# Kernel tuning notes

Hardware: AMD Instinct MI355X
Metric: run time of the kernel (lower is better)

The kernel has to match this reference:

```python
import jax, jax.numpy as jnp
import numpy as np

V, K, C, F = 100000, 64, 3, 16
HID = [64, 64, 64]  # 'large' pca-net hidden widths (config.yaml stand-in)
EPS = 1e-4


def setup_inputs() -> dict:
    key = jax.random.key(0)
    ks = jax.random.split(key, 12)
    inp = {
        "coordinates": jax.random.normal(ks[0], (V, C), jnp.float32),
        "distsq": jax.random.uniform(ks[1], (V, K), jnp.float32),
        "features": jax.random.uniform(ks[2], (V, F), jnp.float32),
        "n_idxs": jax.random.randint(ks[3], (V, K), 0, V, jnp.int32),
    }
    dims = [C * C] + HID + [C * C]
    for i in range(len(dims) - 1):
        fan_in = dims[i]
        inp[f"W{i}"] = jax.random.normal(ks[4 + 2 * i], (dims[i], dims[i + 1]), jnp.float32) / np.sqrt(fan_in)
        inp[f"b{i}"] = jnp.zeros((dims[i + 1],), jnp.float32)
    return inp


def _neighbour_covariance(coordinates, distsq, features, n_idxs):
    # gather neighbour coords/features: [V,K,C], [V,K,F]
    nbc = jnp.take(coordinates, n_idxs, axis=0)
    nbf = jnp.take(features, n_idxs, axis=0)
    # per-neighbour per-feature weights, distsq pre-scaled by 10 in call()
    w = nbf * jnp.exp(-10.0 * distsq)[:, :, None]          # [V,K,F]
    wsum = jnp.sum(w, axis=1) + EPS                         # [V,F]
    mean = jnp.einsum("vkf,vkc->vfc", w, nbc) / wsum[:, :, None]  # [V,F,C]
    # E[x x^T] - mu mu^T (avoids materializing [V,K,F,C] centered diffs)
    m2 = jnp.einsum("vkf,vkc,vkd->vfcd", w, nbc, nbc) / wsum[:, :, None, None]
    cov = m2 - mean[:, :, :, None] * mean[:, :, None, :]    # [V,F,C,C]
    return cov, mean


def reference(coordinates, distsq, features, n_idxs,
              W0, b0, W1, b1, W2, b2, W3, b3):
    cov, mean = _neighbour_covariance(coordinates, distsq, features, n_idxs)
    x = cov.reshape(-1, C * C)                              # [V*F, C^2]
    # per-layer path: ELU on every layer, including the final one
    for Wl, bl in ((W0, b0), (W1, b1), (W2, b2), (W3, b3)):
        x = jax.nn.elu(x @ Wl + bl)
    return x.reshape(-1, F * C * C)                         # [V, F*C^2]
```

## Files before the change

### kernel.cpp

```cpp
#include <hip/hip_runtime.h>
#include <hip/hip_bf16.h>
#include <math.h>

#define NV 100000
#define NK 64
#define NF 16
#define EPS_W 1e-4f
#define WS_NEED ((size_t)NV * 16 * 32)
#define GRID_MLP 3125

typedef __attribute__((ext_vector_type(8))) short bf16x8;
typedef __attribute__((ext_vector_type(4))) float f32x4;

__device__ __forceinline__ unsigned short bfu(float x) {
    return __builtin_bit_cast(unsigned short, (__bf16)x);
}
__device__ __forceinline__ unsigned int pk2(float lo, float hi) {
    float2 t; t.x = lo; t.y = hi;
    __hip_bfloat162 r = __float22bfloat162_rn(t);
    unsigned int u;
    __builtin_memcpy(&u, &r, 4);
    return u;
}
__device__ __forceinline__ float eluf(float x) {
    return x > 0.f ? x : __expf(x) - 1.f;
}

__launch_bounds__(256)
__global__ void cov_kernel(const float* __restrict__ coords,
                           const float* __restrict__ distsq,
                           const float* __restrict__ feats,
                           const int*   __restrict__ nidx,
                           unsigned char* __restrict__ ws)
{
    __shared__ float sEW[16][64];
    __shared__ int   sIX[16][64];
    const int tid = threadIdx.x;
    const int gv  = tid >> 4;
    const int f   = tid & 15;
    const int v   = blockIdx.x * 16 + gv;

    {
        const size_t base = (size_t)v * NK + 4 * f;
        float4 d4 = *(const float4*)(distsq + base);
        int4   i4 = *(const int4*)(nidx + base);
        sEW[gv][4*f+0] = __expf(-10.f * d4.x);
        sEW[gv][4*f+1] = __expf(-10.f * d4.y);
        sEW[gv][4*f+2] = __expf(-10.f * d4.z);
        sEW[gv][4*f+3] = __expf(-10.f * d4.w);
        sIX[gv][4*f+0] = i4.x; sIX[gv][4*f+1] = i4.y;
        sIX[gv][4*f+2] = i4.z; sIX[gv][4*f+3] = i4.w;
    }
    __syncthreads();

    float s = 0.f, m0=0.f,m1=0.f,m2=0.f;
    float q00=0.f,q01=0.f,q02=0.f,q11=0.f,q12=0.f,q22=0.f;

    #pragma unroll 8
    for (int k = 0; k < NK; ++k) {
        int   idx = sIX[gv][k];
        float ew  = sEW[gv][k];
        float w   = feats[(size_t)idx * NF + f] * ew;
        float x = coords[(size_t)idx*3+0];
        float y = coords[(size_t)idx*3+1];
        float z = coords[(size_t)idx*3+2];
        s += w;
        m0 = fmaf(w,x,m0); m1 = fmaf(w,y,m1); m2 = fmaf(w,z,m2);
        float wx=w*x, wy=w*y, wz=w*z;
        q00=fmaf(wx,x,q00); q01=fmaf(wx,y,q01); q02=fmaf(wx,z,q02);
        q11=fmaf(wy,y,q11); q12=fmaf(wy,z,q12); q22=fmaf(wz,z,q22);
    }
    float inv = 1.f / (s + EPS_W);
    float mu0=m0*inv, mu1=m1*inv, mu2=m2*inv;
    float c00=fmaf(-mu0,mu0,q00*inv);
    float c01=fmaf(-mu0,mu1,q01*inv);
    float c02=fmaf(-mu0,mu2,q02*inv);
    float c11=fmaf(-mu1,mu1,q11*inv);
    float c12=fmaf(-mu1,mu2,q12*inv);
    float c22=fmaf(-mu2,mu2,q22*inv);

    uint4 lo, hi;
    lo.x = pk2(c00, c01);
    lo.y = pk2(c02, c01);
    lo.z = pk2(c11, c12);
    lo.w = pk2(c02, c12);
    hi.x = pk2(c22, 1.0f);
    hi.y = 0u; hi.z = 0u; hi.w = 0u;

    uint4* dst = (uint4*)(ws + ((size_t)v * 16 + f) * 32);
    dst[0] = lo;
    dst[1] = hi;
}

__device__ __forceinline__ bf16x8 rdfrag(const short* hb, int c, int g, int kc) {
    int boff = ((kc << 6) + (g << 4)) ^ ((c & 7) << 4);
    return *(const bf16x8*)(hb + c * 64 + (boff >> 1));
}
__device__ __forceinline__ void wrH(short* hb, int c, int g, int t,
                                    unsigned int p01, unsigned int p23) {
    int boff = ((t << 5) + (g << 3)) ^ ((c & 7) << 4);
    uint2 val; val.x = p01; val.y = p23;
    *(uint2*)(hb + c * 64 + (boff >> 1)) = val;
}
__device__ __forceinline__ bf16x8 rdW(const short* sw, int c, int g, int t, int kc) {
    int byte = (t << 11) + (c << 7) + (kc << 6) + (g << 4);
    byte ^= (c & 7) << 4;
    return *(const bf16x8*)((const char*)sw + byte);
}

__launch_bounds__(256, 4)
__global__ void mlp5b_kernel(const unsigned char* __restrict__ ws,
                             const float* __restrict__ W0, const float* __restrict__ b0,
                             const float* __restrict__ W1, const float* __restrict__ b1,
                             const float* __restrict__ W2, const float* __restrict__ b2,
                             const float* __restrict__ W3, const float* __restrict__ b3,
                             float* __restrict__ out)
{
    __shared__ __align__(16) short sW1[4096];
    __shared__ __align__(16) short sW2[4096];
    __shared__ __align__(16) short hbuf[4][1024];

    const int tid  = threadIdx.x;
    const int wid  = tid >> 6;
    const int lane = tid & 63;
    const int c    = lane & 15;
    const int g    = lane >> 4;

    union U8 { short s[8]; bf16x8 v; };

    #pragma unroll
    for (int r = 0; r < 2; ++r) {
        int t = tid + r * 256;
        int j = t & 63, o = t >> 6;
        U8 u1, u2;
        #pragma unroll
        for (int i = 0; i < 8; ++i) {
            u1.s[i] = (short)bfu(W1[(8 * o + i) * 64 + j]);
            u2.s[i] = (short)bfu(W2[(8 * o + i) * 64 + j]);
        }
        int byte = ((j << 7) + (o << 4)) ^ ((j & 7) << 4);
        *(bf16x8*)((char*)sW1 + byte) = u1.v;
        *(bf16x8*)((char*)sW2 + byte) = u2.v;
    }
    __syncthreads();

    bf16x8 w0f[4], w3f[2];
    #pragma unroll
    for (int t = 0; t < 4; ++t) {
        U8 u;
        #pragma unroll
        for (int i = 0; i < 8; ++i) {
            int k = 8 * g + i;
            float val = 0.f;
            if (k < 9)       val = W0[k * 64 + 16 * t + c];
            else if (k == 9) val = b0[16 * t + c];
            u.s[i] = (short)bfu(val);
        }
        w0f[t] = u.v;
    }
    #pragma unroll
    for (int kc = 0; kc < 2; ++kc) {
        U8 u;
        #pragma unroll
        for (int i = 0; i < 8; ++i) {
            int k = 32 * kc + 8 * g + i;
            u.s[i] = (short)bfu(c < 9 ? W3[k * 9 + c] : 0.f);
        }
        w3f[kc] = u.v;
    }
    float b1v[16], b2v[16], b3v[4];
    #pragma unroll
    for (int t = 0; t < 4; ++t)
        #pragma unroll
        for (int r = 0; r < 4; ++r) {
            b1v[4 * t + r] = b1[16 * t + 4 * g + r];
            b2v[4 * t + r] = b2[16 * t + 4 * g + r];
        }
    #pragma unroll
    for (int r = 0; r < 4; ++r)
        b3v[r] = (4 * g + r < 9) ? b3[4 * g + r] : 0.f;

    short* hb = &hbuf[wid][0];
    float* fOut = (float*)hb;

    const int stride = gridDim.x * 4;
    int v = blockIdx.x * 4 + wid;
    if (v >= NV) return;

    const unsigned char* wp = ws + (size_t)v * 512 + (c << 5) + ((g & 1) << 4);
    const size_t wstep = (size_t)stride * 512;
    float* ob = out + (size_t)v * 144;
    const size_t ostep = (size_t)stride * 144;

    bf16x8 bin = *(const bf16x8*)(wp);

    for (; v < NV; v += stride) {
        const unsigned char* wpn = (v + stride < NV) ? (wp + wstep) : wp;
        bf16x8 nb = *(const bf16x8*)(wpn);

        f32x4 A[4];

        #pragma unroll
        for (int t = 0; t < 4; ++t) {
            f32x4 z4 = {0.f, 0.f, 0.f, 0.f};
            A[t] = __builtin_amdgcn_mfma_f32_16x16x32_bf16(w0f[t], bin, z4, 0, 0, 0);
        }
        #pragma unroll
        for (int t = 0; t < 4; ++t)
            wrH(hb, c, g, t, pk2(eluf(A[t][0]), eluf(A[t][1])),
                             pk2(eluf(A[t][2]), eluf(A[t][3])));
        __asm__ volatile("s_waitcnt lgkmcnt(0)" ::: "memory");

        {
            bf16x8 h0 = rdfrag(hb, c, g, 0), h1 = rdfrag(hb, c, g, 1);
            #pragma unroll
            for (int t = 0; t < 4; ++t) {
                bf16x8 wa = rdW(sW1, c, g, t, 0);
                bf16x8 wb = rdW(sW1, c, g, t, 1);
                f32x4 a = { b1v[4*t+0], b1v[4*t+1], b1v[4*t+2], b1v[4*t+3] };
                a = __builtin_amdgcn_mfma_f32_16x16x32_bf16(wa, h0, a, 0, 0, 0);
                a = __builtin_amdgcn_mfma_f32_16x16x32_bf16(wb, h1, a, 0, 0, 0);
                A[t] = a;
            }
            #pragma unroll
            for (int t = 0; t < 4; ++t)
                wrH(hb, c, g, t, pk2(eluf(A[t][0]), eluf(A[t][1])),
                                 pk2(eluf(A[t][2]), eluf(A[t][3])));
        }
        __asm__ volatile("s_waitcnt lgkmcnt(0)" ::: "memory");

        {
            bf16x8 h0 = rdfrag(hb, c, g, 0), h1 = rdfrag(hb, c, g, 1);
            #pragma unroll
            for (int t = 0; t < 4; ++t) {
                bf16x8 wa = rdW(sW2, c, g, t, 0);
                bf16x8 wb = rdW(sW2, c, g, t, 1);
                f32x4 a = { b2v[4*t+0], b2v[4*t+1], b2v[4*t+2], b2v[4*t+3] };
                a = __builtin_amdgcn_mfma_f32_16x16x32_bf16(wa, h0, a, 0, 0, 0);
                a = __builtin_amdgcn_mfma_f32_16x16x32_bf16(wb, h1, a, 0, 0, 0);
                A[t] = a;
            }
            #pragma unroll
            for (int t = 0; t < 4; ++t)
                wrH(hb, c, g, t, pk2(eluf(A[t][0]), eluf(A[t][1])),
                                 pk2(eluf(A[t][2]), eluf(A[t][3])));
        }
        __asm__ volatile("s_waitcnt lgkmcnt(0)" ::: "memory");

        {
            bf16x8 h0 = rdfrag(hb, c, g, 0), h1 = rdfrag(hb, c, g, 1);
            f32x4 a = { b3v[0], b3v[1], b3v[2], b3v[3] };
            a = __builtin_amdgcn_mfma_f32_16x16x32_bf16(w3f[0], h0, a, 0, 0, 0);
            a = __builtin_amdgcn_mfma_f32_16x16x32_bf16(w3f[1], h1, a, 0, 0, 0);
            if (g < 2) {
                fOut[c * 9 + 4 * g + 0] = eluf(a[0]);
                fOut[c * 9 + 4 * g + 1] = eluf(a[1]);
                fOut[c * 9 + 4 * g + 2] = eluf(a[2]);
                fOut[c * 9 + 4 * g + 3] = eluf(a[3]);
            } else if (g == 2) {
                fOut[c * 9 + 8] = eluf(a[0]);
            }
        }
        __asm__ volatile("s_waitcnt lgkmcnt(0)" ::: "memory");

        if (lane < 36) {
            float4 val = *(const float4*)(fOut + lane * 4);
            *(float4*)(ob + lane * 4) = val;
        }
        __asm__ volatile("s_waitcnt lgkmcnt(0)" ::: "memory");

        bin = nb;
        wp = wpn;
        ob += ostep;
    }
}

__launch_bounds__(256, 2)
__global__ void fused_pca_mlp(const float* __restrict__ coords,
                              const float* __restrict__ distsq,
                              const float* __restrict__ feats,
                              const int*   __restrict__ nidx,
                              const float* __restrict__ W0, const float* __restrict__ b0,
                              const float* __restrict__ W1, const float* __restrict__ b1,
                              const float* __restrict__ W2, const float* __restrict__ b2,
                              const float* __restrict__ W3, const float* __restrict__ b3,
                              float* __restrict__ out)
{
    __shared__ __align__(16) float sW0t[64 * 9];
    __shared__ __align__(16) float sW1t[64 * 64];
    __shared__ __align__(16) float sW2t[64 * 64];
    __shared__ __align__(16) float sW3t[9 * 64];
    __shared__ float sB0[64], sB1[64], sB2[64], sB3[9];
    const int tid = threadIdx.x;
    for (int t = tid; t < 64 * 9; t += 256) { int j = t / 9, i = t - j * 9; sW0t[t] = W0[i * 64 + j]; }
    for (int t = tid; t < 64 * 64; t += 256) { int j = t >> 6, i = t & 63; sW1t[t] = W1[i * 64 + j]; }
    for (int t = tid; t < 64 * 64; t += 256) { int j = t >> 6, i = t & 63; sW2t[t] = W2[i * 64 + j]; }
    for (int t = tid; t < 9 * 64; t += 256) { int j = t >> 6, i = t & 63; sW3t[t] = W3[i * 9 + j]; }
    if (tid < 64) { sB0[tid] = b0[tid]; sB1[tid] = b1[tid]; sB2[tid] = b2[tid]; }
    if (tid < 9)  { sB3[tid] = b3[tid]; }
    __syncthreads();
    const int g = tid >> 4, f = tid & 15;
    const int v = blockIdx.x * 16 + g;
    if (v >= NV) return;
    const int* nix = nidx + (size_t)v * NK;
    const float* dsq = distsq + (size_t)v * NK;
    float s = 0.f, m0=0,m1=0,m2=0, q00=0,q01=0,q02=0,q11=0,q12=0,q22=0;
    #pragma unroll 4
    for (int k = 0; k < NK; ++k) {
        int idx = nix[k];
        float ew = __expf(-10.0f * dsq[k]);
        float w = feats[(size_t)idx * NF + f] * ew;
        float x = coords[(size_t)idx*3+0], y = coords[(size_t)idx*3+1], z = coords[(size_t)idx*3+2];
        s += w; m0 = fmaf(w,x,m0); m1 = fmaf(w,y,m1); m2 = fmaf(w,z,m2);
        float wx=w*x, wy=w*y, wz=w*z;
        q00=fmaf(wx,x,q00); q01=fmaf(wx,y,q01); q02=fmaf(wx,z,q02);
        q11=fmaf(wy,y,q11); q12=fmaf(wy,z,q12); q22=fmaf(wz,z,q22);
    }
    float inv = 1.0f/(s+EPS_W), mu0=m0*inv, mu1=m1*inv, mu2=m2*inv;
    float xr[9];
    xr[0]=fmaf(-mu0,mu0,q00*inv); xr[1]=fmaf(-mu0,mu1,q01*inv); xr[2]=fmaf(-mu0,mu2,q02*inv);
    xr[3]=xr[1]; xr[4]=fmaf(-mu1,mu1,q11*inv); xr[5]=fmaf(-mu1,mu2,q12*inv);
    xr[6]=xr[2]; xr[7]=xr[5]; xr[8]=fmaf(-mu2,mu2,q22*inv);
    float h[64], gg[64];
    #pragma unroll
    for (int j = 0; j < 64; ++j) {
        float aa = sB0[j]; const float* wr = sW0t + j * 9;
        #pragma unroll
        for (int i = 0; i < 9; ++i) aa = fmaf(xr[i], wr[i], aa);
        h[j] = eluf(aa);
    }
    #pragma unroll
    for (int j = 0; j < 64; ++j) {
        float aa = sB1[j]; const float4* wr = (const float4*)(sW1t + (j << 6));
        #pragma unroll
        for (int i4 = 0; i4 < 16; ++i4) { float4 wv = wr[i4];
            aa = fmaf(h[4*i4+0],wv.x,aa); aa = fmaf(h[4*i4+1],wv.y,aa);
            aa = fmaf(h[4*i4+2],wv.z,aa); aa = fmaf(h[4*i4+3],wv.w,aa); }
        gg[j] = eluf(aa);
    }
    #pragma unroll
    for (int j = 0; j < 64; ++j) {
        float aa = sB2[j]; const float4* wr = (const float4*)(sW2t + (j << 6));
        #pragma unroll
        for (int i4 = 0; i4 < 16; ++i4) { float4 wv = wr[i4];
            aa = fmaf(gg[4*i4+0],wv.x,aa); aa = fmaf(gg[4*i4+1],wv.y,aa);
            aa = fmaf(gg[4*i4+2],wv.z,aa); aa = fmaf(gg[4*i4+3],wv.w,aa); }
        h[j] = eluf(aa);
    }
    float o[9];
    #pragma unroll
    for (int j = 0; j < 9; ++j) {
        float aa = sB3[j]; const float4* wr = (const float4*)(sW3t + (j << 6));
        #pragma unroll
        for (int i4 = 0; i4 < 16; ++i4) { float4 wv = wr[i4];
            aa = fmaf(h[4*i4+0],wv.x,aa); aa = fmaf(h[4*i4+1],wv.y,aa);
            aa = fmaf(h[4*i4+2],wv.z,aa); aa = fmaf(h[4*i4+3],wv.w,aa); }
        o[j] = eluf(aa);
    }
    float* op = out + ((size_t)v * NF + f) * 9;
    #pragma unroll
    for (int j = 0; j < 9; ++j) op[j] = o[j];
}

extern "C" void kernel_launch(void* const* d_in, const int* in_sizes, int n_in,
                              void* d_out, int out_size, void* d_ws, size_t ws_size,
                              hipStream_t stream) {
    (void)in_sizes; (void)n_in; (void)out_size;
    const float* coords = (const float*)d_in[0];
    const float* distsq = (const float*)d_in[1];
    const float* feats  = (const float*)d_in[2];
    const int*   nidx   = (const int*)d_in[3];
    const float* W0 = (const float*)d_in[4];
    const float* b0 = (const float*)d_in[5];
    const float* W1 = (const float*)d_in[6];
    const float* b1 = (const float*)d_in[7];
    const float* W2 = (const float*)d_in[8];
    const float* b2 = (const float*)d_in[9];
    const float* W3 = (const float*)d_in[10];
    const float* b3 = (const float*)d_in[11];
    float* out = (float*)d_out;

    if (ws_size >= WS_NEED) {
        unsigned char* ws = (unsigned char*)d_ws;
        hipLaunchKernelGGL(cov_kernel, dim3(NV / 16), dim3(256), 0, stream,
                           coords, distsq, feats, nidx, ws);
        hipLaunchKernelGGL(mlp5b_kernel, dim3(GRID_MLP), dim3(256), 0, stream,
                           ws, W0, b0, W1, b1, W2, b2, W3, b3, out);
    } else {
        hipLaunchKernelGGL(fused_pca_mlp, dim3(NV / 16), dim3(256), 0, stream,
                           coords, distsq, feats, nidx,
                           W0, b0, W1, b1, W2, b2, W3, b3, out);
    }
}
```

Baseline: 201.3 us.

## Split neighbour loop across lanes and pass MLP activations via shuffles

The covariance kernel now gives each block 8 vertices and splits each vertex's 64 neighbours between two half-groups of lanes, combining the partial sums with xor shuffles. The point is to double the threads issuing the latency-bound gathers. The MLP kernel no longer writes hidden activations to LDS and reads them back between layers; it rebuilds the MFMA B fragments from the accumulator registers with cross-lane shuffles, removing LDS round trips and waitcnt stalls. The bf16 packing helper also becomes a plain bit-cast combine. The costs are many more shuffle instructions per layer and a duplicated shuffle reduction in the covariance kernel.

```diff
diff --git a/kernel.cpp b/kernel.cpp
--- a/kernel.cpp
+++ b/kernel.cpp
@@ -1,5 +1,4 @@
 #include <hip/hip_runtime.h>
-#include <hip/hip_bf16.h>
 #include <math.h>
 
 #define NV 100000
@@ -16,48 +15,49 @@
     return __builtin_bit_cast(unsigned short, (__bf16)x);
 }
 __device__ __forceinline__ unsigned int pk2(float lo, float hi) {
-    float2 t; t.x = lo; t.y = hi;
-    __hip_bfloat162 r = __float22bfloat162_rn(t);
-    unsigned int u;
-    __builtin_memcpy(&u, &r, 4);
-    return u;
+    return (unsigned int)bfu(lo) | ((unsigned int)bfu(hi) << 16);
 }
 __device__ __forceinline__ float eluf(float x) {
     return x > 0.f ? x : __expf(x) - 1.f;
 }
 
 __launch_bounds__(256)
-__global__ void cov_kernel(const float* __restrict__ coords,
-                           const float* __restrict__ distsq,
-                           const float* __restrict__ feats,
-                           const int*   __restrict__ nidx,
-                           unsigned char* __restrict__ ws)
+__global__ void cov3_kernel(const float* __restrict__ coords,
+                            const float* __restrict__ distsq,
+                            const float* __restrict__ feats,
+                            const int*   __restrict__ nidx,
+                            unsigned char* __restrict__ ws)
 {
-    __shared__ float sEW[16][64];
-    __shared__ int   sIX[16][64];
+    __shared__ float sEW[8][64];
+    __shared__ int   sIX[8][64];
     const int tid = threadIdx.x;
-    const int gv  = tid >> 4;
-    const int f   = tid & 15;
-    const int v   = blockIdx.x * 16 + gv;
-
-    {
-        const size_t base = (size_t)v * NK + 4 * f;
-        float4 d4 = *(const float4*)(distsq + base);
-        int4   i4 = *(const int4*)(nidx + base);
-        sEW[gv][4*f+0] = __expf(-10.f * d4.x);
-        sEW[gv][4*f+1] = __expf(-10.f * d4.y);
-        sEW[gv][4*f+2] = __expf(-10.f * d4.z);
-        sEW[gv][4*f+3] = __expf(-10.f * d4.w);
-        sIX[gv][4*f+0] = i4.x; sIX[gv][4*f+1] = i4.y;
-        sIX[gv][4*f+2] = i4.z; sIX[gv][4*f+3] = i4.w;
+    const int vb  = blockIdx.x * 8;
+
+    #pragma unroll
+    for (int r = 0; r < 2; ++r) {
+        int t  = tid + r * 256;
+        int gv = t >> 6, k = t & 63;
+        float d  = distsq[(size_t)(vb + gv) * NK + k];
+        int   ix = nidx [(size_t)(vb + gv) * NK + k];
+        sEW[gv][k] = __expf(-10.f * d);
+        sIX[gv][k] = ix;
     }
     __syncthreads();
 
-    float s = 0.f, m0=0.f,m1=0.f,m2=0.f;
+    const int lane = tid & 63;
+    const int wid  = tid >> 6;
+    const int f    = lane & 15;
+    const int kh   = (lane >> 4) & 1;
+    const int g2   = lane >> 5;
+    const int gv   = wid * 2 + g2;
+    const int v    = vb + gv;
+
+    float s=0.f, m0=0.f,m1=0.f,m2=0.f;
     float q00=0.f,q01=0.f,q02=0.f,q11=0.f,q12=0.f,q22=0.f;
 
     #pragma unroll 8
-    for (int k = 0; k < NK; ++k) {
+    for (int i = 0; i < 32; ++i) {
+        int   k   = kh * 32 + i;
         int   idx = sIX[gv][k];
         float ew  = sEW[gv][k];
         float w   = feats[(size_t)idx * NF + f] * ew;
@@ -70,55 +70,78 @@
         q00=fmaf(wx,x,q00); q01=fmaf(wx,y,q01); q02=fmaf(wx,z,q02);
         q11=fmaf(wy,y,q11); q12=fmaf(wy,z,q12); q22=fmaf(wz,z,q22);
     }
-    float inv = 1.f / (s + EPS_W);
-    float mu0=m0*inv, mu1=m1*inv, mu2=m2*inv;
-    float c00=fmaf(-mu0,mu0,q00*inv);
-    float c01=fmaf(-mu0,mu1,q01*inv);
-    float c02=fmaf(-mu0,mu2,q02*inv);
-    float c11=fmaf(-mu1,mu1,q11*inv);
-    float c12=fmaf(-mu1,mu2,q12*inv);
-    float c22=fmaf(-mu2,mu2,q22*inv);
-
-    uint4 lo, hi;
-    lo.x = pk2(c00, c01);
-    lo.y = pk2(c02, c01);
-    lo.z = pk2(c11, c12);
-    lo.w = pk2(c02, c12);
-    hi.x = pk2(c22, 1.0f);
-    hi.y = 0u; hi.z = 0u; hi.w = 0u;
-
-    uint4* dst = (uint4*)(ws + ((size_t)v * 16 + f) * 32);
-    dst[0] = lo;
-    dst[1] = hi;
-}
-
-__device__ __forceinline__ bf16x8 rdfrag(const short* hb, int c, int g, int kc) {
-    int boff = ((kc << 6) + (g << 4)) ^ ((c & 7) << 4);
-    return *(const bf16x8*)(hb + c * 64 + (boff >> 1));
-}
-__device__ __forceinline__ void wrH(short* hb, int c, int g, int t,
-                                    unsigned int p01, unsigned int p23) {
-    int boff = ((t << 5) + (g << 3)) ^ ((c & 7) << 4);
-    uint2 val; val.x = p01; val.y = p23;
-    *(uint2*)(hb + c * 64 + (boff >> 1)) = val;
-}
+    s   += __shfl_xor(s,   16);
+    m0  += __shfl_xor(m0,  16);
+    m1  += __shfl_xor(m1,  16);
+    m2  += __shfl_xor(m2,  16);
+    q00 += __shfl_xor(q00, 16);
+    q01 += __shfl_xor(q01, 16);
+    q02 += __shfl_xor(q02, 16);
+    q11 += __shfl_xor(q11, 16);
+    q12 += __shfl_xor(q12, 16);
+    q22 += __shfl_xor(q22, 16);
+
+    if (kh == 0) {
+        float inv = 1.f / (s + EPS_W);
+        float mu0=m0*inv, mu1=m1*inv, mu2=m2*inv;
+        float c00=fmaf(-mu0,mu0,q00*inv);
+        float c01=fmaf(-mu0,mu1,q01*inv);
+        float c02=fmaf(-mu0,mu2,q02*inv);
+        float c11=fmaf(-mu1,mu1,q11*inv);
+        float c12=fmaf(-mu1,mu2,q12*inv);
+        float c22=fmaf(-mu2,mu2,q22*inv);
+
+        uint4 lo, hi;
+        lo.x = pk2(c00, c01);
+        lo.y = pk2(c02, c01);
+        lo.z = pk2(c11, c12);
+        lo.w = pk2(c02, c12);
+        hi.x = pk2(c22, 1.0f);
+        hi.y = 0u; hi.z = 0u; hi.w = 0u;
+
+        uint4* dst = (uint4*)(ws + ((size_t)v * 16 + f) * 32);
+        dst[0] = lo;
+        dst[1] = hi;
+    }
+}
+
 __device__ __forceinline__ bf16x8 rdW(const short* sw, int c, int g, int t, int kc) {
     int byte = (t << 11) + (c << 7) + (kc << 6) + (g << 4);
     byte ^= (c & 7) << 4;
     return *(const bf16x8*)((const char*)sw + byte);
 }
 
+struct B2 { bf16x8 b0, b1; };
+__device__ __forceinline__ B2 d2b(const unsigned int pk_[4][2], int c, int g) {
+    const int srcA = c + ((g & 1) << 5);
+    const int srcB = srcA + 16;
+    const bool hi = (g >> 1) != 0;
+    union { unsigned int u[4]; bf16x8 v; } U0, U1;
+    #pragma unroll
+    for (int m = 0; m < 4; ++m) {
+        int src = (m & 2) ? srcB : srcA;
+        int j   = m & 1;
+        unsigned int e0 = (unsigned int)__shfl((int)pk_[0][j], src);
+        unsigned int o0 = (unsigned int)__shfl((int)pk_[1][j], src);
+        unsigned int e1 = (unsigned int)__shfl((int)pk_[2][j], src);
+        unsigned int o1 = (unsigned int)__shfl((int)pk_[3][j], src);
+        U0.u[m] = hi ? o0 : e0;
+        U1.u[m] = hi ? o1 : e1;
+    }
+    B2 r; r.b0 = U0.v; r.b1 = U1.v; return r;
+}
+
 __launch_bounds__(256, 4)
-__global__ void mlp5b_kernel(const unsigned char* __restrict__ ws,
-                             const float* __restrict__ W0, const float* __restrict__ b0,
-                             const float* __restrict__ W1, const float* __restrict__ b1,
-                             const float* __restrict__ W2, const float* __restrict__ b2,
-                             const float* __restrict__ W3, const float* __restrict__ b3,
-                             float* __restrict__ out)
+__global__ void mlp6_kernel(const unsigned char* __restrict__ ws,
+                            const float* __restrict__ W0, const float* __restrict__ b0,
+                            const float* __restrict__ W1, const float* __restrict__ b1,
+                            const float* __restrict__ W2, const float* __restrict__ b2,
+                            const float* __restrict__ W3, const float* __restrict__ b3,
+                            float* __restrict__ out)
 {
     __shared__ __align__(16) short sW1[4096];
     __shared__ __align__(16) short sW2[4096];
-    __shared__ __align__(16) short hbuf[4][1024];
+    __shared__ __align__(16) float sOut[4][160];
 
     const int tid  = threadIdx.x;
     const int wid  = tid >> 6;
@@ -180,8 +203,7 @@
     for (int r = 0; r < 4; ++r)
         b3v[r] = (4 * g + r < 9) ? b3[4 * g + r] : 0.f;
 
-    short* hb = &hbuf[wid][0];
-    float* fOut = (float*)hb;
+    float* fOut = &sOut[wid][0];
 
     const int stride = gridDim.x * 4;
     int v = blockIdx.x * 4 + wid;
@@ -199,6 +221,7 @@
         bf16x8 nb = *(const bf16x8*)(wpn);
 
         f32x4 A[4];
+        unsigned int pkv[4][2];
 
         #pragma unroll
         for (int t = 0; t < 4; ++t) {
@@ -206,52 +229,48 @@
             A[t] = __builtin_amdgcn_mfma_f32_16x16x32_bf16(w0f[t], bin, z4, 0, 0, 0);
         }
         #pragma unroll
-        for (int t = 0; t < 4; ++t)
-            wrH(hb, c, g, t, pk2(eluf(A[t][0]), eluf(A[t][1])),
-                             pk2(eluf(A[t][2]), eluf(A[t][3])));
-        __asm__ volatile("s_waitcnt lgkmcnt(0)" ::: "memory");
+        for (int t = 0; t < 4; ++t) {
+            pkv[t][0] = pk2(eluf(A[t][0]), eluf(A[t][1]));
+            pkv[t][1] = pk2(eluf(A[t][2]), eluf(A[t][3]));
+        }
+        B2 h = d2b(pkv, c, g);
+
+        #pragma unroll
+        for (int t = 0; t < 4; ++t) {
+            bf16x8 wa = rdW(sW1, c, g, t, 0);
+            bf16x8 wb = rdW(sW1, c, g, t, 1);
+            f32x4 a = { b1v[4*t+0], b1v[4*t+1], b1v[4*t+2], b1v[4*t+3] };
+            a = __builtin_amdgcn_mfma_f32_16x16x32_bf16(wa, h.b0, a, 0, 0, 0);
+            a = __builtin_amdgcn_mfma_f32_16x16x32_bf16(wb, h.b1, a, 0, 0, 0);
+            A[t] = a;
+        }
+        #pragma unroll
+        for (int t = 0; t < 4; ++t) {
+            pkv[t][0] = pk2(eluf(A[t][0]), eluf(A[t][1]));
+            pkv[t][1] = pk2(eluf(A[t][2]), eluf(A[t][3]));
+        }
+        h = d2b(pkv, c, g);
+
+        #pragma unroll
+        for (int t = 0; t < 4; ++t) {
+            bf16x8 wa = rdW(sW2, c, g, t, 0);
+            bf16x8 wb = rdW(sW2, c, g, t, 1);
+            f32x4 a = { b2v[4*t+0], b2v[4*t+1], b2v[4*t+2], b2v[4*t+3] };
+            a = __builtin_amdgcn_mfma_f32_16x16x32_bf16(wa, h.b0, a, 0, 0, 0);
+            a = __builtin_amdgcn_mfma_f32_16x16x32_bf16(wb, h.b1, a, 0, 0, 0);
+            A[t] = a;
+        }
+        #pragma unroll
+        for (int t = 0; t < 4; ++t) {
+            pkv[t][0] = pk2(eluf(A[t][0]), eluf(A[t][1]));
+            pkv[t][1] = pk2(eluf(A[t][2]), eluf(A[t][3]));
+        }
+        h = d2b(pkv, c, g);
 
         {
-            bf16x8 h0 = rdfrag(hb, c, g, 0), h1 = rdfrag(hb, c, g, 1);
-            #pragma unroll
-            for (int t = 0; t < 4; ++t) {
-                bf16x8 wa = rdW(sW1, c, g, t, 0);
-                bf16x8 wb = rdW(sW1, c, g, t, 1);
-                f32x4 a = { b1v[4*t+0], b1v[4*t+1], b1v[4*t+2], b1v[4*t+3] };
-                a = __builtin_amdgcn_mfma_f32_16x16x32_bf16(wa, h0, a, 0, 0, 0);
-                a = __builtin_amdgcn_mfma_f32_16x16x32_bf16(wb, h1, a, 0, 0, 0);
-                A[t] = a;
-            }
-            #pragma unroll
-            for (int t = 0; t < 4; ++t)
-                wrH(hb, c, g, t, pk2(eluf(A[t][0]), eluf(A[t][1])),
-                                 pk2(eluf(A[t][2]), eluf(A[t][3])));
-        }
-        __asm__ volatile("s_waitcnt lgkmcnt(0)" ::: "memory");
-
-        {
-            bf16x8 h0 = rdfrag(hb, c, g, 0), h1 = rdfrag(hb, c, g, 1);
-            #pragma unroll
-            for (int t = 0; t < 4; ++t) {
-                bf16x8 wa = rdW(sW2, c, g, t, 0);
-                bf16x8 wb = rdW(sW2, c, g, t, 1);
-                f32x4 a = { b2v[4*t+0], b2v[4*t+1], b2v[4*t+2], b2v[4*t+3] };
-                a = __builtin_amdgcn_mfma_f32_16x16x32_bf16(wa, h0, a, 0, 0, 0);
-                a = __builtin_amdgcn_mfma_f32_16x16x32_bf16(wb, h1, a, 0, 0, 0);
-                A[t] = a;
-            }
-            #pragma unroll
-            for (int t = 0; t < 4; ++t)
-                wrH(hb, c, g, t, pk2(eluf(A[t][0]), eluf(A[t][1])),
-                                 pk2(eluf(A[t][2]), eluf(A[t][3])));
-        }
-        __asm__ volatile("s_waitcnt lgkmcnt(0)" ::: "memory");
-
-        {
-            bf16x8 h0 = rdfrag(hb, c, g, 0), h1 = rdfrag(hb, c, g, 1);
             f32x4 a = { b3v[0], b3v[1], b3v[2], b3v[3] };
-            a = __builtin_amdgcn_mfma_f32_16x16x32_bf16(w3f[0], h0, a, 0, 0, 0);
-            a = __builtin_amdgcn_mfma_f32_16x16x32_bf16(w3f[1], h1, a, 0, 0, 0);
+            a = __builtin_amdgcn_mfma_f32_16x16x32_bf16(w3f[0], h.b0, a, 0, 0, 0);
+            a = __builtin_amdgcn_mfma_f32_16x16x32_bf16(w3f[1], h.b1, a, 0, 0, 0);
             if (g < 2) {
                 fOut[c * 9 + 4 * g + 0] = eluf(a[0]);
                 fOut[c * 9 + 4 * g + 1] = eluf(a[1]);
@@ -382,9 +401,9 @@
 
     if (ws_size >= WS_NEED) {
         unsigned char* ws = (unsigned char*)d_ws;
-        hipLaunchKernelGGL(cov_kernel, dim3(NV / 16), dim3(256), 0, stream,
+        hipLaunchKernelGGL(cov3_kernel, dim3(NV / 8), dim3(256), 0, stream,
                            coords, distsq, feats, nidx, ws);
-        hipLaunchKernelGGL(mlp5b_kernel, dim3(GRID_MLP), dim3(256), 0, stream,
+        hipLaunchKernelGGL(mlp6_kernel, dim3(GRID_MLP), dim3(256), 0, stream,
                            ws, W0, b0, W1, b1, W2, b2, W3, b3, out);
     } else {
         hipLaunchKernelGGL(fused_pca_mlp, dim3(NV / 16), dim3(256), 0, stream,
```

Result: slower. 214.8 us (+6.7%).
